# Performance work log

Hardware: AMD Instinct MI355X
Metric: run time of the kernel (lower is better)

The kernel has to match this reference:

```python
import jax, jax.numpy as jnp
import numpy as np

NEGATIVE_RATIO = 3.0


def setup_inputs() -> dict:
    key = jax.random.key(0)
    k1, k2, k3, k4, k5 = jax.random.split(key, 5)
    B, N, C = 64, 8732, 81  # batch, num_priors (SSD300), num_classes (COCO)
    pred_conf = jax.random.normal(k1, (B, N, C), dtype=jnp.float32)
    pred_loc = jax.random.normal(k2, (B, N, 4), dtype=jnp.float32)
    labels = jax.random.randint(k3, (B, N), 1, C)
    is_pos = jax.random.uniform(k4, (B, N)) < 0.03
    labels = jnp.where(is_pos, labels, 0)
    labels = labels.at[:, 0].set(1)  # guarantee >=1 positive per image
    gt_conf = jax.nn.one_hot(labels, C, dtype=jnp.float32)
    pos = (labels > 0)[..., None].astype(jnp.float32)
    gt_loc = jax.random.normal(k5, (B, N, 4), dtype=jnp.float32) * pos
    return {"pred_conf": pred_conf, "pred_loc": pred_loc,
            "gt_conf": gt_conf, "gt_loc": gt_loc}


def reference(pred_conf, pred_loc, gt_conf, gt_loc):
    B, N, _ = pred_conf.shape
    # ----- conf loss: cross entropy against one-hot gt -----
    conf_loss = -(jax.nn.log_softmax(pred_conf, axis=-1) * gt_conf).sum(-1)  # [B, N]
    pos_mask = gt_conf[:, :, 0] == 0  # non-background priors
    num_pos = pos_mask.sum(-1).astype(pred_conf.dtype)  # [B]
    pos_conf_loss = jnp.where(pos_mask, conf_loss, 0.0).sum(-1)  # [B]
    # ----- hard negative mining: keep losses strictly above k-th largest negative loss -----
    num_neg = num_pos * NEGATIVE_RATIO  # [B], float
    neg_loss = jnp.where(pos_mask, 0.0, conf_loss)  # zero out positives
    sorted_desc = -jnp.sort(-neg_loss, axis=-1)  # descending per row
    k = jnp.clip(num_neg.astype(jnp.int32), 0, N - 1)  # [B]
    thresh = jnp.take_along_axis(sorted_desc, k[:, None], axis=-1)  # [B, 1]
    neg_mask = neg_loss > thresh  # only true on negatives (pos entries are 0)
    neg_conf_loss = jnp.where(neg_mask, conf_loss, 0.0).sum(-1)  # [B]
    conf_total = pos_conf_loss / num_pos + neg_conf_loss / num_neg  # [B]
    # ----- loc loss: smooth L1 on priors with nonzero gt_loc -----
    loc_mask = gt_loc != 0  # [B, N, 4]
    num_pos_loc = jnp.any(loc_mask, axis=-1).sum(-1).astype(pred_loc.dtype)  # [B]
    diff = jnp.abs(pred_loc - gt_loc)
    smooth_l1 = jnp.where(diff < 1.0, 0.5 * diff * diff, diff - 0.5)
    loc_total = jnp.where(loc_mask, smooth_l1, 0.0).sum((-1, -2)) / num_pos_loc  # [B]
    return (conf_total + loc_total).mean()
```

## Files before the change

### kernel.cpp

```cpp
#include <hip/hip_runtime.h>
#include <math.h>

#define BB 64
#define NN 8732
#define CC 81
#define ROWS_PER_BLOCK 128

__global__ void init_kernel(unsigned* acc) {
    int i = threadIdx.x;
    if (i < 4 * BB) acc[i] = 0u;
}

__global__ __launch_bounds__(256) void conf_kernel(
        const float* __restrict__ pred_conf,
        const float* __restrict__ gt_conf,
        float* __restrict__ neg_loss,
        int* __restrict__ num_pos,
        float* __restrict__ pos_sum) {
    __shared__ float lbuf[ROWS_PER_BLOCK * CC + 8];
    __shared__ int   s_cnt;
    __shared__ float s_sum;

    const int b       = blockIdx.y;
    const int rowBase = blockIdx.x * ROWS_PER_BLOCK;
    const int nrows   = min(ROWS_PER_BLOCK, NN - rowBase);
    const size_t TOTF = (size_t)BB * NN * CC;

    if (threadIdx.x == 0) { s_cnt = 0; s_sum = 0.f; }

    const size_t seg = ((size_t)b * NN + rowBase) * CC;
    const int    cnt = nrows * CC;
    const size_t a0  = seg & ~(size_t)3;
    const int  shift = (int)(seg - a0);
    const int   tot4 = (shift + cnt + 3) >> 2;

    const float4* g4 = (const float4*)(pred_conf + a0);
    float4*       l4 = (float4*)lbuf;
    for (int i = threadIdx.x; i < tot4; i += 256) {
        size_t gf = a0 + 4 * (size_t)i;
        if (gf + 4 <= TOTF) {
            l4[i] = g4[i];
        } else {
            #pragma unroll
            for (int c = 0; c < 4; ++c)
                lbuf[4 * i + c] = (gf + c < TOTF) ? pred_conf[gf + c] : 0.f;
        }
    }
    __syncthreads();

    const int r = threadIdx.x >> 1;
    const int h = threadIdx.x & 1;
    if (r < nrows) {
        const float* row = lbuf + shift + r * CC;
        const int c0 = h ? 41 : 0;
        const int c1 = h ? CC : 41;

        const size_t gbase = ((size_t)b * NN + rowBase + r) * CC;
        const float gt0 = gt_conf[gbase];

        float m = -1e30f;
        for (int c = c0; c < c1; ++c) m = fmaxf(m, row[c]);
        m = fmaxf(m, __shfl_xor(m, 1, 64));

        float e = 0.f;
        for (int c = c0; c < c1; ++c) e += __expf(row[c] - m);
        e += __shfl_xor(e, 1, 64);

        const bool pos = (gt0 == 0.f);
        float x_sel;
        if (pos) {
            float d = 0.f;
            for (int c = c0; c < c1; ++c) d += gt_conf[gbase + c] * row[c];
            d += __shfl_xor(d, 1, 64);
            x_sel = d;
        } else {
            x_sel = row[0];
        }

        const float loss = m + __logf(e) - x_sel;
        if (h == 0) {
            neg_loss[(size_t)b * NN + rowBase + r] = pos ? 0.f : loss;
            if (pos) {
                atomicAdd(&s_cnt, 1);
                atomicAdd(&s_sum, loss);
            }
        }
    }
    __syncthreads();
    if (threadIdx.x == 0 && s_cnt) {
        atomicAdd(&num_pos[b], s_cnt);
        atomicAdd(&pos_sum[b], s_sum);
    }
}

__global__ __launch_bounds__(256) void loc_kernel(
        const float* __restrict__ pred_loc,
        const float* __restrict__ gt_loc,
        float* __restrict__ loc_cnt,
        float* __restrict__ loc_sum) {
    const int b = blockIdx.y;
    const float4* pl = (const float4*)pred_loc;
    const float4* gl = (const float4*)gt_loc;

    float sum = 0.f, cnt = 0.f;
    for (int j = 0; j < 8; ++j) {
        int n = blockIdx.x * 2048 + j * 256 + threadIdx.x;
        if (n < NN) {
            size_t idx = (size_t)b * NN + n;
            float4 p = pl[idx];
            float4 g = gl[idx];
            bool any = false;
            float pv[4] = {p.x, p.y, p.z, p.w};
            float gv[4] = {g.x, g.y, g.z, g.w};
            #pragma unroll
            for (int c = 0; c < 4; ++c) {
                if (gv[c] != 0.f) {
                    any = true;
                    float d = fabsf(pv[c] - gv[c]);
                    sum += (d < 1.f) ? 0.5f * d * d : d - 0.5f;
                }
            }
            if (any) cnt += 1.f;
        }
    }
    for (int o = 32; o; o >>= 1) {
        sum += __shfl_down(sum, o, 64);
        cnt += __shfl_down(cnt, o, 64);
    }
    __shared__ float s_sum, s_cnt;
    if (threadIdx.x == 0) { s_sum = 0.f; s_cnt = 0.f; }
    __syncthreads();
    if ((threadIdx.x & 63) == 0) {
        atomicAdd(&s_sum, sum);
        atomicAdd(&s_cnt, cnt);
    }
    __syncthreads();
    if (threadIdx.x == 0) {
        atomicAdd(&loc_sum[b], s_sum);
        atomicAdd(&loc_cnt[b], s_cnt);
    }
}

__global__ __launch_bounds__(256) void select_kernel(
        const float* __restrict__ neg_loss,
        const int*   __restrict__ num_pos,
        const float* __restrict__ pos_sum,
        const float* __restrict__ loc_cnt,
        const float* __restrict__ loc_sum,
        float* __restrict__ per_b) {
    const int b   = blockIdx.x;
    const int tid = threadIdx.x;
    const int lane = tid & 63;
    __shared__ unsigned vals[NN];
    __shared__ unsigned hist[256];
    __shared__ unsigned scan[256];
    __shared__ unsigned sh_prefix, sh_r;
    __shared__ float    s_part[4];

    for (int i = tid; i < NN; i += 256)
        vals[i] = __float_as_uint(neg_loss[(size_t)b * NN + i]);

    const int np = num_pos[b];
    const int k  = min(3 * np, NN - 1);
    if (tid == 0) { sh_prefix = 0u; sh_r = (unsigned)k; }
    __syncthreads();

    unsigned prefix_mask = 0u;
    for (int p = 3; p >= 0; --p) {
        const unsigned pref = sh_prefix;
        const unsigned r    = sh_r;
        hist[tid] = 0u;
        __syncthreads();

        for (int i0 = 0; i0 < NN; i0 += 256) {
            const int i = i0 + tid;
            const bool act = (i < NN) && ((vals[i] & prefix_mask) == pref);
            const unsigned v   = act ? vals[i] : 0u;
            const unsigned bin = (v >> (8 * p)) & 255u;
            unsigned long long mm = __ballot(act);
            #pragma unroll
            for (int bit = 0; bit < 8; ++bit) {
                unsigned long long s = __ballot(act && ((bin >> bit) & 1u));
                mm &= ((bin >> bit) & 1u) ? s : ~s;
            }
            if (act && ((mm & ((1ull << lane) - 1ull)) == 0ull))
                atomicAdd(&hist[bin], (unsigned)__popcll(mm));
        }
        __syncthreads();

        scan[tid] = hist[tid];
        __syncthreads();
        for (int off = 1; off < 256; off <<= 1) {
            unsigned add = (tid + off < 256) ? scan[tid + off] : 0u;
            __syncthreads();
            scan[tid] += add;
            __syncthreads();
        }
        const unsigned Si  = scan[tid];
        const unsigned Si1 = (tid < 255) ? scan[tid + 1] : 0u;
        __syncthreads();
        if (Si1 <= r && r < Si) {
            sh_r = r - Si1;
            sh_prefix = pref | ((unsigned)tid << (8 * p));
        }
        __syncthreads();
        prefix_mask |= 0xFFu << (8 * p);
    }

    const float thresh = __uint_as_float(sh_prefix);
    float s = 0.f;
    for (int i = tid; i < NN; i += 256) {
        float v = __uint_as_float(vals[i]);
        if (v > thresh) s += v;
    }
    for (int o = 32; o; o >>= 1) s += __shfl_down(s, o, 64);
    if (lane == 0) s_part[tid >> 6] = s;
    __syncthreads();
    if (tid == 0) {
        float neg_sum = s_part[0] + s_part[1] + s_part[2] + s_part[3];
        float npf = (float)np;
        per_b[b] = pos_sum[b] / npf + neg_sum / (3.0f * npf) + loc_sum[b] / loc_cnt[b];
    }
}

__global__ void finalize_kernel(const float* __restrict__ per_b, float* __restrict__ out) {
    float v = (threadIdx.x < BB) ? per_b[threadIdx.x] : 0.f;
    for (int o = 32; o; o >>= 1) v += __shfl_down(v, o, 64);
    if (threadIdx.x == 0) out[0] = v * (1.0f / BB);
}

extern "C" void kernel_launch(void* const* d_in, const int* in_sizes, int n_in,
                              void* d_out, int out_size, void* d_ws, size_t ws_size,
                              hipStream_t stream) {
    const float* pred_conf = (const float*)d_in[0];
    const float* pred_loc  = (const float*)d_in[1];
    const float* gt_conf   = (const float*)d_in[2];
    const float* gt_loc    = (const float*)d_in[3];

    float* neg      = (float*)d_ws;
    int*   num_pos  = (int*)(neg + (size_t)BB * NN);
    float* pos_sum  = (float*)(num_pos + BB);
    float* loc_cnt  = pos_sum + BB;
    float* loc_sum  = loc_cnt + BB;
    float* per_b    = loc_sum + BB;

    init_kernel<<<1, 256, 0, stream>>>((unsigned*)num_pos);

    dim3 cgrid((NN + ROWS_PER_BLOCK - 1) / ROWS_PER_BLOCK, BB);
    conf_kernel<<<cgrid, 256, 0, stream>>>(pred_conf, gt_conf, neg, num_pos, pos_sum);

    dim3 lgrid((NN + 2047) / 2048, BB);
    loc_kernel<<<lgrid, 256, 0, stream>>>(pred_loc, gt_loc, loc_cnt, loc_sum);

    select_kernel<<<BB, 256, 0, stream>>>(neg, num_pos, pos_sum, loc_cnt, loc_sum, per_b);

    finalize_kernel<<<1, 64, 0, stream>>>(per_b, (float*)d_out);
}
```

Measured before the change: 434.2 us.

## Fuse conf and loc kernels, use four threads per row, shuffle-based scan

Merges the loc smooth-L1 kernel into the conf kernel as extra blocks, and folds the finalize step into select_kernel via an atomic add on the output, which removes two launches. The conf path now uses 64 rows per block with four threads per row, holding values in registers, which cuts per-thread serial work and shared-memory use so more blocks can be resident. The select kernel's 256-wide log-step shared-memory scan, with its many barriers, is replaced by a single-wavefront shuffle scan over groups of four bins. The atomic final sum adds float ordering nondeterminism.

```diff
diff --git a/kernel.cpp b/kernel.cpp
--- a/kernel.cpp
+++ b/kernel.cpp
@@ -4,29 +4,77 @@
 #define BB 64
 #define NN 8732
 #define CC 81
-#define ROWS_PER_BLOCK 128
-
-__global__ void init_kernel(unsigned* acc) {
+#define ROWS 64
+#define CBX ((NN + ROWS - 1) / ROWS)
+#define LBX 5
+
+__global__ void init_kernel(unsigned* acc, float* out) {
     int i = threadIdx.x;
     if (i < 4 * BB) acc[i] = 0u;
-}
-
-__global__ __launch_bounds__(256) void conf_kernel(
+    if (i == 0) out[0] = 0.f;
+}
+
+__global__ __launch_bounds__(256) void fused_kernel(
         const float* __restrict__ pred_conf,
         const float* __restrict__ gt_conf,
+        const float* __restrict__ pred_loc,
+        const float* __restrict__ gt_loc,
         float* __restrict__ neg_loss,
         int* __restrict__ num_pos,
-        float* __restrict__ pos_sum) {
-    __shared__ float lbuf[ROWS_PER_BLOCK * CC + 8];
+        float* __restrict__ pos_sum,
+        float* __restrict__ loc_cnt,
+        float* __restrict__ loc_sum) {
+    const int b   = blockIdx.y;
+    const int tid = threadIdx.x;
+
+    if (blockIdx.x >= CBX) {
+        const int lb = blockIdx.x - CBX;
+        const float4* pl = (const float4*)pred_loc;
+        const float4* gl = (const float4*)gt_loc;
+        float sum = 0.f, cnt = 0.f;
+        #pragma unroll
+        for (int j = 0; j < 8; ++j) {
+            int n = lb * 2048 + j * 256 + tid;
+            if (n < NN) {
+                size_t idx = (size_t)b * NN + n;
+                float4 p = pl[idx];
+                float4 g = gl[idx];
+                bool any = false;
+                float pv[4] = {p.x, p.y, p.z, p.w};
+                float gv[4] = {g.x, g.y, g.z, g.w};
+                #pragma unroll
+                for (int c = 0; c < 4; ++c) {
+                    if (gv[c] != 0.f) {
+                        any = true;
+                        float d = fabsf(pv[c] - gv[c]);
+                        sum += (d < 1.f) ? 0.5f * d * d : d - 0.5f;
+                    }
+                }
+                if (any) cnt += 1.f;
+            }
+        }
+        for (int o = 32; o; o >>= 1) {
+            sum += __shfl_down(sum, o, 64);
+            cnt += __shfl_down(cnt, o, 64);
+        }
+        __shared__ float ls_sum, ls_cnt;
+        if (tid == 0) { ls_sum = 0.f; ls_cnt = 0.f; }
+        __syncthreads();
+        if ((tid & 63) == 0) { atomicAdd(&ls_sum, sum); atomicAdd(&ls_cnt, cnt); }
+        __syncthreads();
+        if (tid == 0) { atomicAdd(&loc_sum[b], ls_sum); atomicAdd(&loc_cnt[b], ls_cnt); }
+        return;
+    }
+
+    __shared__ float lbuf[ROWS * CC + 8];
     __shared__ int   s_cnt;
     __shared__ float s_sum;
 
-    const int b       = blockIdx.y;
-    const int rowBase = blockIdx.x * ROWS_PER_BLOCK;
-    const int nrows   = min(ROWS_PER_BLOCK, NN - rowBase);
+    const int rowBase = blockIdx.x * ROWS;
+    const int nrows   = min(ROWS, NN - rowBase);
     const size_t TOTF = (size_t)BB * NN * CC;
 
-    if (threadIdx.x == 0) { s_cnt = 0; s_sum = 0.f; }
+    if (tid == 0) { s_cnt = 0; s_sum = 0.f; }
 
     const size_t seg = ((size_t)b * NN + rowBase) * CC;
     const int    cnt = nrows * CC;
@@ -36,7 +84,7 @@
 
     const float4* g4 = (const float4*)(pred_conf + a0);
     float4*       l4 = (float4*)lbuf;
-    for (int i = threadIdx.x; i < tot4; i += 256) {
+    for (int i = tid; i < tot4; i += 256) {
         size_t gf = a0 + 4 * (size_t)i;
         if (gf + 4 <= TOTF) {
             l4[i] = g4[i];
@@ -48,96 +96,54 @@
     }
     __syncthreads();
 
-    const int r = threadIdx.x >> 1;
-    const int h = threadIdx.x & 1;
+    const int r = tid >> 2;
+    const int h = tid & 3;
     if (r < nrows) {
+        const int c0 = h * 20 + (h > 0 ? 1 : 0);
+        const int nc = (h == 0) ? 21 : 20;
         const float* row = lbuf + shift + r * CC;
-        const int c0 = h ? 41 : 0;
-        const int c1 = h ? CC : 41;
-
         const size_t gbase = ((size_t)b * NN + rowBase + r) * CC;
         const float gt0 = gt_conf[gbase];
 
-        float m = -1e30f;
-        for (int c = c0; c < c1; ++c) m = fmaxf(m, row[c]);
+        float v[21];
+        #pragma unroll
+        for (int j = 0; j < 21; ++j)
+            v[j] = (j < nc) ? row[c0 + j] : -1e30f;
+
+        float m = v[0];
+        #pragma unroll
+        for (int j = 1; j < 21; ++j) m = fmaxf(m, v[j]);
         m = fmaxf(m, __shfl_xor(m, 1, 64));
+        m = fmaxf(m, __shfl_xor(m, 2, 64));
 
         float e = 0.f;
-        for (int c = c0; c < c1; ++c) e += __expf(row[c] - m);
+        #pragma unroll
+        for (int j = 0; j < 21; ++j) e += __expf(v[j] - m);
         e += __shfl_xor(e, 1, 64);
+        e += __shfl_xor(e, 2, 64);
 
         const bool pos = (gt0 == 0.f);
-        float x_sel;
+        float x_sel = v[0];
         if (pos) {
             float d = 0.f;
-            for (int c = c0; c < c1; ++c) d += gt_conf[gbase + c] * row[c];
+            #pragma unroll
+            for (int j = 0; j < 21; ++j)
+                if (j < nc) d += gt_conf[gbase + c0 + j] * v[j];
             d += __shfl_xor(d, 1, 64);
+            d += __shfl_xor(d, 2, 64);
             x_sel = d;
-        } else {
-            x_sel = row[0];
         }
 
         const float loss = m + __logf(e) - x_sel;
         if (h == 0) {
             neg_loss[(size_t)b * NN + rowBase + r] = pos ? 0.f : loss;
-            if (pos) {
-                atomicAdd(&s_cnt, 1);
-                atomicAdd(&s_sum, loss);
-            }
-        }
-    }
-    __syncthreads();
-    if (threadIdx.x == 0 && s_cnt) {
+            if (pos) { atomicAdd(&s_cnt, 1); atomicAdd(&s_sum, loss); }
+        }
+    }
+    __syncthreads();
+    if (tid == 0 && s_cnt) {
         atomicAdd(&num_pos[b], s_cnt);
         atomicAdd(&pos_sum[b], s_sum);
-    }
-}
-
-__global__ __launch_bounds__(256) void loc_kernel(
-        const float* __restrict__ pred_loc,
-        const float* __restrict__ gt_loc,
-        float* __restrict__ loc_cnt,
-        float* __restrict__ loc_sum) {
-    const int b = blockIdx.y;
-    const float4* pl = (const float4*)pred_loc;
-    const float4* gl = (const float4*)gt_loc;
-
-    float sum = 0.f, cnt = 0.f;
-    for (int j = 0; j < 8; ++j) {
-        int n = blockIdx.x * 2048 + j * 256 + threadIdx.x;
-        if (n < NN) {
-            size_t idx = (size_t)b * NN + n;
-            float4 p = pl[idx];
-            float4 g = gl[idx];
-            bool any = false;
-            float pv[4] = {p.x, p.y, p.z, p.w};
-            float gv[4] = {g.x, g.y, g.z, g.w};
-            #pragma unroll
-            for (int c = 0; c < 4; ++c) {
-                if (gv[c] != 0.f) {
-                    any = true;
-                    float d = fabsf(pv[c] - gv[c]);
-                    sum += (d < 1.f) ? 0.5f * d * d : d - 0.5f;
-                }
-            }
-            if (any) cnt += 1.f;
-        }
-    }
-    for (int o = 32; o; o >>= 1) {
-        sum += __shfl_down(sum, o, 64);
-        cnt += __shfl_down(cnt, o, 64);
-    }
-    __shared__ float s_sum, s_cnt;
-    if (threadIdx.x == 0) { s_sum = 0.f; s_cnt = 0.f; }
-    __syncthreads();
-    if ((threadIdx.x & 63) == 0) {
-        atomicAdd(&s_sum, sum);
-        atomicAdd(&s_cnt, cnt);
-    }
-    __syncthreads();
-    if (threadIdx.x == 0) {
-        atomicAdd(&loc_sum[b], s_sum);
-        atomicAdd(&loc_cnt[b], s_cnt);
     }
 }
 
@@ -147,16 +153,16 @@
         const float* __restrict__ pos_sum,
         const float* __restrict__ loc_cnt,
         const float* __restrict__ loc_sum,
-        float* __restrict__ per_b) {
-    const int b   = blockIdx.x;
-    const int tid = threadIdx.x;
+        float* __restrict__ out) {
+    const int b    = blockIdx.x;
+    const int tid  = threadIdx.x;
     const int lane = tid & 63;
     __shared__ unsigned vals[NN];
     __shared__ unsigned hist[256];
-    __shared__ unsigned scan[256];
     __shared__ unsigned sh_prefix, sh_r;
     __shared__ float    s_part[4];
 
+    #pragma unroll 4
     for (int i = tid; i < NN; i += 256)
         vals[i] = __float_as_uint(neg_loss[(size_t)b * NN + i]);
 
@@ -188,20 +194,29 @@
         }
         __syncthreads();
 
-        scan[tid] = hist[tid];
-        __syncthreads();
-        for (int off = 1; off < 256; off <<= 1) {
-            unsigned add = (tid + off < 256) ? scan[tid + off] : 0u;
-            __syncthreads();
-            scan[tid] += add;
-            __syncthreads();
-        }
-        const unsigned Si  = scan[tid];
-        const unsigned Si1 = (tid < 255) ? scan[tid + 1] : 0u;
-        __syncthreads();
-        if (Si1 <= r && r < Si) {
-            sh_r = r - Si1;
-            sh_prefix = pref | ((unsigned)tid << (8 * p));
+        if (tid < 64) {
+            const unsigned h0 = hist[4 * tid + 0];
+            const unsigned h1 = hist[4 * tid + 1];
+            const unsigned h2 = hist[4 * tid + 2];
+            const unsigned h3 = hist[4 * tid + 3];
+            unsigned T = h0 + h1 + h2 + h3;
+            #pragma unroll
+            for (int off = 1; off < 64; off <<= 1) {
+                unsigned t2 = __shfl_down(T, off, 64);
+                if (tid + off < 64) T += t2;
+            }
+            unsigned Tn = __shfl_down(T, 1, 64);
+            if (tid == 63) Tn = 0u;
+            const unsigned S4 = Tn, S3 = S4 + h3, S2 = S3 + h2, S1 = S2 + h1, S0 = S1 + h0;
+            int bin = -1; unsigned Slo = 0u;
+            if      (S1 <= r && r < S0) { bin = 4 * tid + 0; Slo = S1; }
+            else if (S2 <= r && r < S1) { bin = 4 * tid + 1; Slo = S2; }
+            else if (S3 <= r && r < S2) { bin = 4 * tid + 2; Slo = S3; }
+            else if (S4 <= r && r < S3) { bin = 4 * tid + 3; Slo = S4; }
+            if (bin >= 0) {
+                sh_r = r - Slo;
+                sh_prefix = pref | ((unsigned)bin << (8 * p));
+            }
         }
         __syncthreads();
         prefix_mask |= 0xFFu << (8 * p);
@@ -209,6 +224,7 @@
 
     const float thresh = __uint_as_float(sh_prefix);
     float s = 0.f;
+    #pragma unroll 4
     for (int i = tid; i < NN; i += 256) {
         float v = __uint_as_float(vals[i]);
         if (v > thresh) s += v;
@@ -219,14 +235,9 @@
     if (tid == 0) {
         float neg_sum = s_part[0] + s_part[1] + s_part[2] + s_part[3];
         float npf = (float)np;
-        per_b[b] = pos_sum[b] / npf + neg_sum / (3.0f * npf) + loc_sum[b] / loc_cnt[b];
-    }
-}
-
-__global__ void finalize_kernel(const float* __restrict__ per_b, float* __restrict__ out) {
-    float v = (threadIdx.x < BB) ? per_b[threadIdx.x] : 0.f;
-    for (int o = 32; o; o >>= 1) v += __shfl_down(v, o, 64);
-    if (threadIdx.x == 0) out[0] = v * (1.0f / BB);
+        float res = pos_sum[b] / npf + neg_sum / (3.0f * npf) + loc_sum[b] / loc_cnt[b];
+        atomicAdd(out, res * (1.0f / BB));
+    }
 }
 
 extern "C" void kernel_launch(void* const* d_in, const int* in_sizes, int n_in,
@@ -242,17 +253,13 @@
     float* pos_sum  = (float*)(num_pos + BB);
     float* loc_cnt  = pos_sum + BB;
     float* loc_sum  = loc_cnt + BB;
-    float* per_b    = loc_sum + BB;
-
-    init_kernel<<<1, 256, 0, stream>>>((unsigned*)num_pos);
-
-    dim3 cgrid((NN + ROWS_PER_BLOCK - 1) / ROWS_PER_BLOCK, BB);
-    conf_kernel<<<cgrid, 256, 0, stream>>>(pred_conf, gt_conf, neg, num_pos, pos_sum);
-
-    dim3 lgrid((NN + 2047) / 2048, BB);
-    loc_kernel<<<lgrid, 256, 0, stream>>>(pred_loc, gt_loc, loc_cnt, loc_sum);
-
-    select_kernel<<<BB, 256, 0, stream>>>(neg, num_pos, pos_sum, loc_cnt, loc_sum, per_b);
-
-    finalize_kernel<<<1, 64, 0, stream>>>(per_b, (float*)d_out);
-}
+
+    init_kernel<<<1, 256, 0, stream>>>((unsigned*)num_pos, (float*)d_out);
+
+    dim3 fgrid(CBX + LBX, BB);
+    fused_kernel<<<fgrid, 256, 0, stream>>>(pred_conf, gt_conf, pred_loc, gt_loc,
+                                            neg, num_pos, pos_sum, loc_cnt, loc_sum);
+
+    select_kernel<<<BB, 256, 0, stream>>>(neg, num_pos, pos_sum, loc_cnt, loc_sum,
+                                          (float*)d_out);
+}
```

Result: faster. 425.1 us (-2.1%).
